# Optimization experiments

Hardware: AMD Instinct MI355X
Metric: run time of the kernel (lower is better)

The kernel has to match this reference:

```python
import jax, jax.numpy as jnp
import numpy as np

H = 64  # LSTM hidden size ('unit' in the torch module)

def _lstm_params(k, scale):
    k1, k2, k3 = jax.random.split(k, 3)
    wih = jax.random.uniform(k1, (4 * H, 1), minval=-scale, maxval=scale, dtype=jnp.float32)
    whh = jax.random.uniform(k2, (4 * H, H), minval=-scale, maxval=scale, dtype=jnp.float32)
    b = jax.random.uniform(k3, (4 * H,), minval=-scale, maxval=scale, dtype=jnp.float32)  # b_ih + b_hh folded
    return wih, whh, b

def _linear_params(k, out_d, in_d):
    k1, k2 = jax.random.split(k)
    s = 1.0 / np.sqrt(in_d)
    w = jax.random.uniform(k1, (out_d, in_d), minval=-s, maxval=s, dtype=jnp.float32)
    b = jax.random.uniform(k2, (out_d,), minval=-s, maxval=s, dtype=jnp.float32)
    return w, b

def setup_inputs():
    key = jax.random.key(0)
    ks = jax.random.split(key, 16)
    B, T, A = 4096, 32, 6
    s = 1.0 / np.sqrt(H)
    inp = {
        'x0': jax.random.normal(ks[0], (B, T, 1), dtype=jnp.float32),
        'x1': jax.random.normal(ks[1], (B, T, 1), dtype=jnp.float32),
        'x2': jax.random.normal(ks[2], (B, T, 1), dtype=jnp.float32),
        's2': jax.random.normal(ks[3], (B, 3), dtype=jnp.float32),
    }
    for name, k in [('q00', ks[4]), ('q01', ks[5]), ('i00', ks[6]), ('i01', ks[7]), ('i02', ks[8])]:
        wih, whh, b = _lstm_params(k, s)
        inp[name + '_wih'], inp[name + '_whh'], inp[name + '_b'] = wih, whh, b
    inp['q03_w'], inp['q03_b'] = _linear_params(ks[9], H, 3)
    inp['q1_w'], inp['q1_b'] = _linear_params(ks[10], H, 4 * H)
    inp['q2_w'], inp['q2_b'] = _linear_params(ks[11], A, H)
    inp['i03_w'], inp['i03_b'] = _linear_params(ks[12], H, 3)
    inp['i1_w'], inp['i1_b'] = _linear_params(ks[13], H, 4 * H)
    inp['i2_w'], inp['i2_b'] = _linear_params(ks[14], A, H)
    return inp

def _lstm_hn(x, wih, whh, b):
    # x: [B,T,1] -> final hidden state h_T: [B,H]. PyTorch gate order: i, f, g, o.
    B = x.shape[0]
    gx = jnp.einsum('bti,gi->btg', x, wih) + b        # [B,T,4H], input part precomputed
    gx = jnp.swapaxes(gx, 0, 1)                        # [T,B,4H]
    h0 = jnp.zeros((B, H), x.dtype)
    def step(carry, g):
        h, c = carry
        g = g + h @ whh.T
        i, f, gg, o = jnp.split(g, 4, axis=-1)
        c = jax.nn.sigmoid(f) * c + jax.nn.sigmoid(i) * jnp.tanh(gg)
        h = jax.nn.sigmoid(o) * jnp.tanh(c)
        return (h, c), None
    (h, _), _ = jax.lax.scan(step, (h0, h0), gx)
    return h

def reference(x0, x1, x2, s2,
              q00_wih, q00_whh, q00_b, q01_wih, q01_whh, q01_b,
              i00_wih, i00_whh, i00_b, i01_wih, i01_whh, i01_b, i02_wih, i02_whh, i02_b,
              q03_w, q03_b, q1_w, q1_b, q2_w, q2_b,
              i03_w, i03_b, i1_w, i1_b, i2_w, i2_b):
    # q branch (NOTE: original code applies q01 to BOTH x1 and x2 -- reproduced faithfully)
    hn0 = _lstm_hn(x0, q00_wih, q00_whh, q00_b)
    hn1 = _lstm_hn(x1, q01_wih, q01_whh, q01_b)
    hn2 = _lstm_hn(x2, q01_wih, q01_whh, q01_b)
    hn3 = jax.nn.relu(s2 @ q03_w.T + q03_b)
    hq = jnp.concatenate([hn0, hn1, hn2, hn3], axis=1)  # [B,4H]
    q = jax.nn.relu(hq @ q1_w.T + q1_b)
    # i branch
    hn0 = _lstm_hn(x0, i00_wih, i00_whh, i00_b)
    hn1 = _lstm_hn(x1, i01_wih, i01_whh, i01_b)
    hn2 = _lstm_hn(x2, i02_wih, i02_whh, i02_b)
    hn3 = jax.nn.relu(s2 @ i03_w.T + i03_b)
    hi = jnp.concatenate([hn0, hn1, hn2, hn3], axis=1)
    i = jax.nn.relu(hi @ i1_w.T + i1_b)
    i = jax.nn.relu(i @ i2_w.T + i2_b)                   # [B,A]
    return (q @ q2_w.T + q2_b, jax.nn.log_softmax(i, axis=1), i)
```

## Files before the change

kernel.cpp:

```cpp
#include <hip/hip_runtime.h>

#define BTOT 4096
#define TS 32

typedef __attribute__((ext_vector_type(8))) short bfrag;
typedef __attribute__((ext_vector_type(4))) float f32x4;

#define S1 (-1.44269504089f)
#define S2 (-2.88539008178f)

__device__ __forceinline__ short f2bf(float f){
  union { float f; unsigned u; } v; v.f = f;
  unsigned r = v.u + 0x7FFFu + ((v.u >> 16) & 1u);
  return (short)(r >> 16);
}
__device__ __forceinline__ float bf2f(short s){
  union { unsigned u; float f; } v; v.u = ((unsigned)(unsigned short)s) << 16; return v.f;
}

struct LstmP {
  const float* x[6];
  const float* wih[6];
  const float* whh[6];
  const float* bias[6];
  float* hout;
};

struct EpiP {
  const float* hout;
  const float* s2;
  const float* w03[2]; const float* b03[2];
  const float* w1[2];  const float* b1[2];
  const float* w2[2];  const float* b2[2];
  float* out;
};

__global__ __launch_bounds__(128) void lstm6(LstmP p){
  const int run = blockIdx.y;
  const int b0 = blockIdx.x * 16;
  const int t = threadIdx.x;
  const int w = t >> 6, lane = t & 63;
  const int i16 = lane & 15, q = lane >> 4;

  __shared__ bfrag hb[2][16*9];
  __shared__ float xs[16*33];

  const float* __restrict__ whh = p.whh[run];

  bfrag B[4][2][2];
  float wihv[4][2], bv[4][2];
#pragma unroll
  for (int g = 0; g < 4; ++g){
    const float sg = (g == 2) ? S2 : S1;
#pragma unroll
    for (int ss = 0; ss < 2; ++ss){
      const int n = 64*g + 16*(2*w + ss) + i16;
      const float* wr = whh + n*64;
#pragma unroll
      for (int kf = 0; kf < 2; ++kf){
        const float* src = wr + 32*kf + 8*q;
        bfrag bb;
#pragma unroll
        for (int j = 0; j < 8; ++j) bb[j] = f2bf(src[j] * sg);
        B[g][ss][kf] = bb;
      }
      wihv[g][ss] = p.wih[run][n] * sg;
      bv[g][ss]   = p.bias[run][n] * sg;
    }
  }
  {
    const float* x = p.x[run] + (size_t)b0 * TS;
    for (int i = t; i < 16*TS; i += 128) xs[(i>>5)*33 + (i&31)] = x[i];
    int* hz = (int*)&hb[0][0];
    for (int i = t; i < 576; i += 128) hz[i] = 0;
  }
  __syncthreads();

  float c[2][4] = {{0,0,0,0},{0,0,0,0}};
  float hlast[2][4];

  for (int s = 0; s < TS; ++s){
    const bfrag* hh = hb[s & 1];
    short* wh = (short*)hb[(s+1) & 1];
    const int af = i16*9 + q;
    bfrag ah0 = hh[af];
    bfrag ah1 = hh[af + 4];
    float xm[4];
#pragma unroll
    for (int r = 0; r < 4; ++r) xm[r] = xs[(4*q + r)*33 + s];

#pragma unroll
    for (int ss = 0; ss < 2; ++ss){
      f32x4 acc[4];
#pragma unroll
      for (int g = 0; g < 4; ++g){
#pragma unroll
        for (int r = 0; r < 4; ++r) acc[g][r] = fmaf(xm[r], wihv[g][ss], bv[g][ss]);
        acc[g] = __builtin_amdgcn_mfma_f32_16x16x32_bf16(ah0, B[g][ss][0], acc[g], 0,0,0);
        acc[g] = __builtin_amdgcn_mfma_f32_16x16x32_bf16(ah1, B[g][ss][1], acc[g], 0,0,0);
      }
#pragma unroll
      for (int r = 0; r < 4; ++r){
        float ei = __builtin_amdgcn_exp2f(acc[0][r]);
        float ef = __builtin_amdgcn_exp2f(acc[1][r]);
        float eg = __builtin_amdgcn_exp2f(acc[2][r]);
        float eo = __builtin_amdgcn_exp2f(acc[3][r]);
        float pf = 1.0f + ef;
        float D1 = (1.0f + eg) * (1.0f + ei);
        float num = fmaf(c[ss][r], D1, (1.0f - eg) * pf);
        float cc = num * __builtin_amdgcn_rcpf(pf * D1);
        c[ss][r] = cc;
        float ec = __builtin_amdgcn_exp2f(cc * S2);
        float hv = (1.0f - ec) * __builtin_amdgcn_rcpf((1.0f + ec) * (1.0f + eo));
        hlast[ss][r] = hv;
        wh[(4*q + r)*72 + 16*(2*w + ss) + i16] = f2bf(hv);
      }
    }
    __syncthreads();
  }

#pragma unroll
  for (int ss = 0; ss < 2; ++ss)
#pragma unroll
    for (int r = 0; r < 4; ++r){
      int m = 4*q + r, j = 16*(2*w + ss) + i16;
      p.hout[((size_t)run*BTOT + b0 + m)*64 + j] = hlast[ss][r];
    }
}

__global__ __launch_bounds__(256) void epilogue(EpiP p){
  const int br = blockIdx.y;
  const int b0 = blockIdx.x * 16;
  const int t = threadIdx.x;
  const int wave = t >> 6, lane = t & 63;
  const int i16 = lane & 15, q = lane >> 4;

  __shared__ bfrag hqv_hi[16*33], hqv_lo[16*33];
  __shared__ float qv[16*66];
  __shared__ float iv[16][6];

  const float* hbase = p.hout + (size_t)br*3*BTOT*64;
  {
    short4* dh = (short4*)hqv_hi;
    short4* dl = (short4*)hqv_lo;
    for (int i = t; i < 768; i += 256){
      int run = i >> 8, ii = i & 255;
      int e = ii >> 4, j4 = ii & 15;
      float4 v = *(const float4*)(hbase + ((size_t)run*BTOT + b0 + e)*64 + j4*4);
      short4 h, l;
      short x0 = f2bf(v.x); h.x = x0; l.x = f2bf(v.x - bf2f(x0));
      short x1 = f2bf(v.y); h.y = x1; l.y = f2bf(v.y - bf2f(x1));
      short x2 = f2bf(v.z); h.z = x2; l.z = f2bf(v.z - bf2f(x2));
      short x3 = f2bf(v.w); h.w = x3; l.w = f2bf(v.w - bf2f(x3));
      int o4 = e*66 + run*16 + j4;
      dh[o4] = h;
      dl[o4] = l;
    }
  }
  {
    short* sh = (short*)hqv_hi;
    short* sl = (short*)hqv_lo;
    const float* w03 = p.w03[br];
    const float* b03 = p.b03[br];
    for (int i = t; i < 1024; i += 256){
      int e = i >> 6, jj = i & 63;
      const float* s2r = p.s2 + (size_t)(b0 + e)*3;
      float v = fmaf(s2r[0], w03[jj*3+0],
                fmaf(s2r[1], w03[jj*3+1],
                fmaf(s2r[2], w03[jj*3+2], b03[jj])));
      v = fmaxf(v, 0.0f);
      int off = e*264 + 192 + jj;
      short hi = f2bf(v);
      sh[off] = hi;
      sl[off] = f2bf(v - bf2f(hi));
    }
  }
  __syncthreads();

  {
    const int n = 16*wave + i16;
    const float* w1r = p.w1[br] + (size_t)n*256;
    f32x4 acc;
    { float bb = p.b1[br][n]; acc[0]=bb; acc[1]=bb; acc[2]=bb; acc[3]=bb; }
#pragma unroll
    for (int ks = 0; ks < 8; ++ks){
      bfrag ah = hqv_hi[i16*33 + 4*ks + q];
      bfrag al = hqv_lo[i16*33 + 4*ks + q];
      const float* src = w1r + 32*ks + 8*q;
      bfrag bh, bl;
#pragma unroll
      for (int j = 0; j < 8; ++j){
        float f = src[j];
        short hi = f2bf(f);
        bh[j] = hi;
        bl[j] = f2bf(f - bf2f(hi));
      }
      acc = __builtin_amdgcn_mfma_f32_16x16x32_bf16(ah, bh, acc, 0,0,0);
      acc = __builtin_amdgcn_mfma_f32_16x16x32_bf16(al, bh, acc, 0,0,0);
      acc = __builtin_amdgcn_mfma_f32_16x16x32_bf16(ah, bl, acc, 0,0,0);
    }
#pragma unroll
    for (int r = 0; r < 4; ++r)
      qv[(4*q + r)*66 + n] = fmaxf(acc[r], 0.0f);
  }
  __syncthreads();

  if (t < 96){
    int e = t / 6, a = t % 6;
    const float* w2r = p.w2[br] + a*64;
    const float* qe = qv + e*66;
    float acc2 = p.b2[br][a];
#pragma unroll 8
    for (int k = 0; k < 64; ++k) acc2 = fmaf(qe[k], w2r[k], acc2);
    int b = b0 + e;
    if (br == 0){
      p.out[(size_t)b*6 + a] = acc2;
    } else {
      float v = fmaxf(acc2, 0.0f);
      iv[e][a] = v;
      p.out[(size_t)2*BTOT*6 + (size_t)b*6 + a] = v;
    }
  }
  __syncthreads();
  if (br == 1 && t < 16){
    float m = iv[t][0];
    for (int a2 = 1; a2 < 6; ++a2) m = fmaxf(m, iv[t][a2]);
    float ss = 0.0f;
    for (int a2 = 0; a2 < 6; ++a2) ss += __expf(iv[t][a2] - m);
    float ls = __logf(ss);
    int b = b0 + t;
    for (int a2 = 0; a2 < 6; ++a2)
      p.out[(size_t)BTOT*6 + (size_t)b*6 + a2] = iv[t][a2] - m - ls;
  }
}

extern "C" void kernel_launch(void* const* d_in, const int* in_sizes, int n_in,
                              void* d_out, int out_size, void* d_ws, size_t ws_size,
                              hipStream_t stream) {
  const float* x0 = (const float*)d_in[0];
  const float* x1 = (const float*)d_in[1];
  const float* x2 = (const float*)d_in[2];
  const float* s2 = (const float*)d_in[3];

  LstmP lp;
  lp.x[0]=x0; lp.x[1]=x1; lp.x[2]=x2; lp.x[3]=x0; lp.x[4]=x1; lp.x[5]=x2;
  const int wbase[6] = {4, 7, 7, 10, 13, 16};
  for (int r = 0; r < 6; ++r){
    lp.wih[r]  = (const float*)d_in[wbase[r]+0];
    lp.whh[r]  = (const float*)d_in[wbase[r]+1];
    lp.bias[r] = (const float*)d_in[wbase[r]+2];
  }
  lp.hout = (float*)d_ws;

  lstm6<<<dim3(BTOT/16, 6), 128, 0, stream>>>(lp);

  EpiP ep;
  ep.hout = (const float*)d_ws;
  ep.s2 = s2;
  ep.w03[0]=(const float*)d_in[19]; ep.b03[0]=(const float*)d_in[20];
  ep.w1 [0]=(const float*)d_in[21]; ep.b1 [0]=(const float*)d_in[22];
  ep.w2 [0]=(const float*)d_in[23]; ep.b2 [0]=(const float*)d_in[24];
  ep.w03[1]=(const float*)d_in[25]; ep.b03[1]=(const float*)d_in[26];
  ep.w1 [1]=(const float*)d_in[27]; ep.b1 [1]=(const float*)d_in[28];
  ep.w2 [1]=(const float*)d_in[29]; ep.b2 [1]=(const float*)d_in[30];
  ep.out = (float*)d_out;

  epilogue<<<dim3(BTOT/16, 2), 256, 0, stream>>>(ep);
}
```

Baseline: 209.6 us.

## Run each LSTM tile on a single wave and drop per-step barriers

The LSTM recurrence kernel now launches 64-thread blocks, so one wave computes all 64 hidden columns of a 16-row batch tile instead of splitting them across two waves. Because the shared hidden-state buffer is now private to one wave, the __syncthreads after every timestep is removed. The cost is a doubled register footprint for the recurrent weight fragments and a per-wave serial chain twice as long. It also halves the number of resident waves, which reduces latency hiding across the MFMA and transcendental dependency chains.

```diff
diff --git a/kernel.cpp b/kernel.cpp
--- a/kernel.cpp
+++ b/kernel.cpp
@@ -35,11 +35,10 @@
   float* out;
 };
 
-__global__ __launch_bounds__(128) void lstm6(LstmP p){
+__global__ __launch_bounds__(64) void lstm6(LstmP p){
   const int run = blockIdx.y;
   const int b0 = blockIdx.x * 16;
-  const int t = threadIdx.x;
-  const int w = t >> 6, lane = t & 63;
+  const int lane = threadIdx.x;
   const int i16 = lane & 15, q = lane >> 4;
 
   __shared__ bfrag hb[2][16*9];
@@ -47,14 +46,14 @@
 
   const float* __restrict__ whh = p.whh[run];
 
-  bfrag B[4][2][2];
-  float wihv[4][2], bv[4][2];
+  bfrag B[4][4][2];
+  float wihv[4][4], bv[4][4];
 #pragma unroll
   for (int g = 0; g < 4; ++g){
     const float sg = (g == 2) ? S2 : S1;
 #pragma unroll
-    for (int ss = 0; ss < 2; ++ss){
-      const int n = 64*g + 16*(2*w + ss) + i16;
+    for (int jt = 0; jt < 4; ++jt){
+      const int n = 64*g + 16*jt + i16;
       const float* wr = whh + n*64;
 #pragma unroll
       for (int kf = 0; kf < 2; ++kf){
@@ -62,22 +61,26 @@
         bfrag bb;
 #pragma unroll
         for (int j = 0; j < 8; ++j) bb[j] = f2bf(src[j] * sg);
-        B[g][ss][kf] = bb;
-      }
-      wihv[g][ss] = p.wih[run][n] * sg;
-      bv[g][ss]   = p.bias[run][n] * sg;
+        B[g][jt][kf] = bb;
+      }
+      wihv[g][jt] = p.wih[run][n] * sg;
+      bv[g][jt]   = p.bias[run][n] * sg;
     }
   }
   {
     const float* x = p.x[run] + (size_t)b0 * TS;
-    for (int i = t; i < 16*TS; i += 128) xs[(i>>5)*33 + (i&31)] = x[i];
+    for (int i = lane; i < 16*TS; i += 64) xs[(i>>5)*33 + (i&31)] = x[i];
     int* hz = (int*)&hb[0][0];
-    for (int i = t; i < 576; i += 128) hz[i] = 0;
-  }
-  __syncthreads();
-
-  float c[2][4] = {{0,0,0,0},{0,0,0,0}};
-  float hlast[2][4];
+    for (int i = lane; i < 576; i += 64) hz[i] = 0;
+  }
+  __syncthreads();
+
+  float c[4][4];
+#pragma unroll
+  for (int jt = 0; jt < 4; ++jt)
+#pragma unroll
+    for (int r = 0; r < 4; ++r) c[jt][r] = 0.0f;
+  float hlast[4][4];
 
   for (int s = 0; s < TS; ++s){
     const bfrag* hh = hb[s & 1];
@@ -90,14 +93,14 @@
     for (int r = 0; r < 4; ++r) xm[r] = xs[(4*q + r)*33 + s];
 
 #pragma unroll
-    for (int ss = 0; ss < 2; ++ss){
+    for (int jt = 0; jt < 4; ++jt){
       f32x4 acc[4];
 #pragma unroll
       for (int g = 0; g < 4; ++g){
 #pragma unroll
-        for (int r = 0; r < 4; ++r) acc[g][r] = fmaf(xm[r], wihv[g][ss], bv[g][ss]);
-        acc[g] = __builtin_amdgcn_mfma_f32_16x16x32_bf16(ah0, B[g][ss][0], acc[g], 0,0,0);
-        acc[g] = __builtin_amdgcn_mfma_f32_16x16x32_bf16(ah1, B[g][ss][1], acc[g], 0,0,0);
+        for (int r = 0; r < 4; ++r) acc[g][r] = fmaf(xm[r], wihv[g][jt], bv[g][jt]);
+        acc[g] = __builtin_amdgcn_mfma_f32_16x16x32_bf16(ah0, B[g][jt][0], acc[g], 0,0,0);
+        acc[g] = __builtin_amdgcn_mfma_f32_16x16x32_bf16(ah1, B[g][jt][1], acc[g], 0,0,0);
       }
 #pragma unroll
       for (int r = 0; r < 4; ++r){
@@ -107,24 +110,23 @@
         float eo = __builtin_amdgcn_exp2f(acc[3][r]);
         float pf = 1.0f + ef;
         float D1 = (1.0f + eg) * (1.0f + ei);
-        float num = fmaf(c[ss][r], D1, (1.0f - eg) * pf);
+        float num = fmaf(c[jt][r], D1, (1.0f - eg) * pf);
         float cc = num * __builtin_amdgcn_rcpf(pf * D1);
-        c[ss][r] = cc;
+        c[jt][r] = cc;
         float ec = __builtin_amdgcn_exp2f(cc * S2);
         float hv = (1.0f - ec) * __builtin_amdgcn_rcpf((1.0f + ec) * (1.0f + eo));
-        hlast[ss][r] = hv;
-        wh[(4*q + r)*72 + 16*(2*w + ss) + i16] = f2bf(hv);
-      }
-    }
-    __syncthreads();
-  }
-
-#pragma unroll
-  for (int ss = 0; ss < 2; ++ss)
+        hlast[jt][r] = hv;
+        wh[(4*q + r)*72 + 16*jt + i16] = f2bf(hv);
+      }
+    }
+  }
+
+#pragma unroll
+  for (int jt = 0; jt < 4; ++jt)
 #pragma unroll
     for (int r = 0; r < 4; ++r){
-      int m = 4*q + r, j = 16*(2*w + ss) + i16;
-      p.hout[((size_t)run*BTOT + b0 + m)*64 + j] = hlast[ss][r];
+      int m = 4*q + r, j = 16*jt + i16;
+      p.hout[((size_t)run*BTOT + b0 + m)*64 + j] = hlast[jt][r];
     }
 }
 
@@ -252,7 +254,7 @@
   }
   lp.hout = (float*)d_ws;
 
-  lstm6<<<dim3(BTOT/16, 6), 128, 0, stream>>>(lp);
+  lstm6<<<dim3(BTOT/16, 6), 64, 0, stream>>>(lp);
 
   EpiP ep;
   ep.hout = (const float*)d_ws;
```

After: 242.8 us. 15.8% more time.
